# Performance work log

Measured on AMD Instinct MI355X. Metric: run time of the kernel, lower is better.

The kernel has to match this reference:

```python
import math
import jax, jax.numpy as jnp
import numpy as np

# ---- DeepSeek-V2-Lite decoder layer config ----
H = 16            # num_attention_heads
D_NOPE = 128      # qk_nope_head_dim
D_ROPE = 64       # qk_rope_head_dim
D_Q = D_NOPE + D_ROPE  # q_head_dim = 192
D_V = 128         # v_head_dim
KV_RANK = 512     # kv_lora_rank
HID = 2048        # hidden_size
INTER = 10944     # intermediate_size (dense MLP)
MAX_POS = 8192
BASE = 10000.0
FACTOR = 40.0     # yarn scaling factor
ORIG_MAX = 4096
BETA_FAST, BETA_SLOW = 32, 1
MSCALE = 0.707
MSCALE_ALL = 0.707
EPS = 1e-6


def _yarn_cos_sin():
    # DeepseekV2LiteYarnRotaryEmbedding._set_cos_sin_cache
    dim = D_ROPE
    ar = np.arange(0, dim, 2, dtype=np.float32) / dim
    freq_extra = 1.0 / BASE ** ar
    freq_inter = 1.0 / (FACTOR * BASE ** ar)

    def corr_dim(num_rot):
        return dim * math.log(ORIG_MAX / (num_rot * 2 * math.pi)) / (2 * math.log(BASE))

    low = max(math.floor(corr_dim(BETA_FAST)), 0)
    high = min(math.ceil(corr_dim(BETA_SLOW)), dim - 1)
    hi = high + 0.001 if low == high else high
    ramp = np.clip((np.arange(dim // 2, dtype=np.float32) - low) / (hi - low), 0.0, 1.0)
    inv_freq_mask = 1.0 - ramp
    inv_freq = freq_inter * (1 - inv_freq_mask) + freq_extra * inv_freq_mask
    t = np.arange(MAX_POS, dtype=np.float32)
    freqs = np.outer(t, inv_freq)

    def get_mscale(s, m):
        return 1.0 if s <= 1 else 0.1 * m * math.log(s) + 1.0

    ms = get_mscale(FACTOR, MSCALE) / get_mscale(FACTOR, MSCALE_ALL)
    emb = np.concatenate([freqs, freqs], axis=-1)
    return jnp.asarray(np.cos(emb) * ms, jnp.float32), jnp.asarray(np.sin(emb) * ms, jnp.float32)

COS_CACHE, SIN_CACHE = _yarn_cos_sin()  # [MAX_POS, D_ROPE]


def _rms(x, w):
    return x * jax.lax.rsqrt(jnp.mean(x * x, axis=-1, keepdims=True) + EPS) * w


def _deinterleave(x):
    # view(..., d//2, 2).transpose(-1, -2).reshape(..., d)
    d = x.shape[-1]
    return x.reshape(x.shape[:-1] + (d // 2, 2)).swapaxes(-1, -2).reshape(x.shape)


def _apply_rope(x, cos, sin):
    x = _deinterleave(x)
    d = x.shape[-1]
    x1, x2 = x[..., : d // 2], x[..., d // 2:]
    return x * cos + jnp.concatenate([-x2, x1], axis=-1) * sin


def _decoder_layer(hidden_states, position_ids, Wq, Wkva, w_kvln, Wkvb, Wo, Wg, Wu, Wd, w_ln1, w_ln2):
    b, s, _ = hidden_states.shape
    dt = hidden_states.dtype

    # ---- attention block ----
    residual = hidden_states
    x = _rms(hidden_states, w_ln1)

    q = (x @ Wq.T).reshape(b, s, H, D_Q)                 # [b,s,h,192]
    q_nope, q_pe = q[..., :D_NOPE], q[..., D_NOPE:]

    ckv = x @ Wkva.T                                     # [b,s,576]
    c, k_pe = ckv[..., :KV_RANK], ckv[..., KV_RANK:][:, :, None, :]  # [b,s,512],[b,s,1,64]
    kv = (_rms(c, w_kvln) @ Wkvb.T).reshape(b, s, H, D_NOPE + D_V)
    k_nope, v = kv[..., :D_NOPE], kv[..., D_NOPE:]

    cos = COS_CACHE[position_ids][:, :, None, :].astype(dt)  # unsqueeze_dim=2
    sin = SIN_CACHE[position_ids][:, :, None, :].astype(dt)
    q_pe = _apply_rope(q_pe, cos, sin)
    k_pe = _apply_rope(k_pe, cos, sin)

    qf = jnp.concatenate([q_nope, q_pe], axis=-1)                          # [b,s,h,192]
    kf = jnp.concatenate([k_nope, jnp.broadcast_to(k_pe, (b, s, H, D_ROPE))], axis=-1)

    scale = D_Q ** -0.5
    scores = jnp.einsum('bqhd,bkhd->bhqk', qf, kf) * scale
    causal = jnp.tril(jnp.ones((s, s), dtype=bool))
    scores = jnp.where(causal, scores, jnp.finfo(scores.dtype).min)
    probs = jax.nn.softmax(scores, axis=-1)
    attn = jnp.einsum('bhqk,bkhd->bqhd', probs, v).reshape(b, s, H * D_V)
    x = residual + attn @ Wo.T

    # ---- MLP block (SwiGLU) ----
    residual = x
    y = _rms(x, w_ln2)
    x = residual + (jax.nn.silu(y @ Wg.T) * (y @ Wu.T)) @ Wd.T
    return x


def setup_inputs() -> dict:
    key = jax.random.key(0)
    ks = jax.random.split(key, 12)
    B, S = 2, 2048
    sd = 0.02
    inp = {
        'hidden_states': jax.random.normal(ks[0], (B, S, HID), jnp.float32),
        'position_ids': jnp.broadcast_to(jnp.arange(S, dtype=jnp.int32), (B, S)),
        'Wq': jax.random.normal(ks[1], (H * D_Q, HID), jnp.float32) * sd,
        'Wkva': jax.random.normal(ks[2], (KV_RANK + D_ROPE, HID), jnp.float32) * sd,
        'w_kvln': jnp.ones((KV_RANK,), jnp.float32),
        'Wkvb': jax.random.normal(ks[3], (H * (D_NOPE + D_V), KV_RANK), jnp.float32) * sd,
        'Wo': jax.random.normal(ks[4], (HID, H * D_V), jnp.float32) * sd,
        'Wg': jax.random.normal(ks[5], (INTER, HID), jnp.float32) * sd,
        'Wu': jax.random.normal(ks[6], (INTER, HID), jnp.float32) * sd,
        'Wd': jax.random.normal(ks[7], (HID, INTER), jnp.float32) * sd,
        'w_ln1': jnp.ones((HID,), jnp.float32),
        'w_ln2': jnp.ones((HID,), jnp.float32),
    }
    return inp


def reference(hidden_states, position_ids, Wq, Wkva, w_kvln, Wkvb, Wo, Wg, Wu, Wd, w_ln1, w_ln2):
    return _decoder_layer(hidden_states, position_ids, Wq, Wkva, w_kvln, Wkvb, Wo, Wg, Wu, Wd, w_ln1, w_ln2)
```

## Files before the change

### kernel.cpp

```cpp
#include <hip/hip_runtime.h>
#include <hip/hip_bf16.h>
#include <math.h>


typedef short short8 __attribute__((ext_vector_type(8)));
typedef short short4v __attribute__((ext_vector_type(4)));
typedef float f32x4 __attribute__((ext_vector_type(4)));

static __device__ __forceinline__ float bf2f(ushort u) {
  union { uint i; float f; } v; v.i = ((uint)u) << 16; return v.f;
}
static __device__ __forceinline__ ushort f2bf(float x) {
  union { float f; uint i; } v; v.f = x;
  uint r = v.i + 0x7fffu + ((v.i >> 16) & 1u);
  return (ushort)(r >> 16);
}

static __device__ __forceinline__ void glds16(const ushort* g, ushort* l) {
  __builtin_amdgcn_global_load_lds(
      (const __attribute__((address_space(1))) unsigned int*)g,
      (__attribute__((address_space(3))) unsigned int*)l, 16, 0, 0);
}

__global__ __launch_bounds__(256)
void cvt_bf16(const float* __restrict__ in, ushort* __restrict__ out, int n8) {
  int i = blockIdx.x * 256 + threadIdx.x;
  if (i >= n8) return;
  float4 a = ((const float4*)in)[2 * i];
  float4 b = ((const float4*)in)[2 * i + 1];
  short8 o;
  o[0] = (short)f2bf(a.x); o[1] = (short)f2bf(a.y);
  o[2] = (short)f2bf(a.z); o[3] = (short)f2bf(a.w);
  o[4] = (short)f2bf(b.x); o[5] = (short)f2bf(b.y);
  o[6] = (short)f2bf(b.z); o[7] = (short)f2bf(b.w);
  ((short8*)out)[i] = o;
}

__global__ __launch_bounds__(256)
void rms_bf16(const float* __restrict__ in, int istride, int width, float inv_w,
              const float* __restrict__ w, ushort* __restrict__ out, int ostride) {
  const int row = blockIdx.x;
  const float* x = in + (size_t)row * istride;
  float ss = 0.f;
  for (int i = threadIdx.x; i < width; i += 256) { float v = x[i]; ss += v * v; }
#pragma unroll
  for (int off = 32; off > 0; off >>= 1) ss += __shfl_xor(ss, off);
  __shared__ float red[4];
  if ((threadIdx.x & 63) == 0) red[threadIdx.x >> 6] = ss;
  __syncthreads();
  float tot = red[0] + red[1] + red[2] + red[3];
  float scale = rsqrtf(tot * inv_w + 1e-6f);
  ushort* o = out + (size_t)row * ostride;
  for (int i = threadIdx.x; i < width; i += 256) o[i] = f2bf(x[i] * scale * w[i]);
}

template<int EPI>
__global__ __launch_bounds__(256, 2)
void gemm_as(const ushort* __restrict__ A, const ushort* __restrict__ B,
             void* __restrict__ Cv, const void* __restrict__ resv,
             int M, int N, int K) {
  __shared__ ushort As[128 * 32];
  __shared__ ushort Bs[128 * 32];
  const int tid = threadIdx.x;
  const int wave = tid >> 6, lane = tid & 63;
  const int m0 = blockIdx.x * 128, n0 = blockIdx.y * 128;
  const int lm = lane & 15, quad = lane >> 4;
  const int wm = (wave & 1) * 64, wn = (wave >> 1) * 64;

  const int srow = wave * 32 + (lane >> 2);
  const int scol = (lane & 3) * 8;
  const ushort* gA0 = A + (size_t)(m0 + srow) * K + scol;
  const ushort* gA1 = A + (size_t)(m0 + srow + 16) * K + scol;
  int br0 = n0 + srow;      if (br0 > N - 1) br0 = N - 1;
  int br1 = n0 + srow + 16; if (br1 > N - 1) br1 = N - 1;
  const ushort* gB0 = B + (size_t)br0 * K + scol;
  const ushort* gB1 = B + (size_t)br1 * K + scol;
  ushort* lA0 = &As[(wave * 32) * 32];
  ushort* lA1 = &As[(wave * 32 + 16) * 32];
  ushort* lB0 = &Bs[(wave * 32) * 32];
  ushort* lB1 = &Bs[(wave * 32 + 16) * 32];

  f32x4 acc[4][4];
  const f32x4 z4 = {0.f, 0.f, 0.f, 0.f};
#pragma unroll
  for (int i = 0; i < 4; ++i)
#pragma unroll
    for (int j = 0; j < 4; ++j) acc[i][j] = z4;

  for (int k0 = 0; k0 < K; k0 += 32) {
    glds16(gA0 + k0, lA0);
    glds16(gA1 + k0, lA1);
    glds16(gB0 + k0, lB0);
    glds16(gB1 + k0, lB1);
    __syncthreads();

    short8 afr[4], bfr[4];
#pragma unroll
    for (int mt = 0; mt < 4; ++mt)
      afr[mt] = *(const short8*)&As[(wm + mt * 16 + lm) * 32 + quad * 8];
#pragma unroll
    for (int nt = 0; nt < 4; ++nt)
      bfr[nt] = *(const short8*)&Bs[(wn + nt * 16 + lm) * 32 + quad * 8];
#pragma unroll
    for (int mt = 0; mt < 4; ++mt)
#pragma unroll
      for (int nt = 0; nt < 4; ++nt)
        acc[mt][nt] = __builtin_amdgcn_mfma_f32_16x16x32_bf16(
            afr[mt], bfr[nt], acc[mt][nt], 0, 0, 0);
    __syncthreads();
  }

#pragma unroll
  for (int mt = 0; mt < 4; ++mt) {
#pragma unroll
    for (int r = 0; r < 4; ++r) {
      const int grow = m0 + wm + mt * 16 + quad * 4 + r;
#pragma unroll
      for (int nt = 0; nt < 4; ++nt) {
        const int gcol = n0 + wn + nt * 16 + lm;
        if (gcol < N) {
          const size_t idx = (size_t)grow * N + gcol;
          float vacc = acc[mt][nt][r];
          if (EPI == 0) {
            ((ushort*)Cv)[idx] = f2bf(vacc);
          } else if (EPI == 1) {
            ((float*)Cv)[idx] = vacc;
          } else if (EPI == 2) {
            ((float*)Cv)[idx] = vacc + ((const float*)resv)[idx];
          } else {
            float gv = bf2f(((const ushort*)resv)[idx]);
            ((ushort*)Cv)[idx] = f2bf(gv / (1.f + expf(-gv)) * vacc);
          }
        }
      }
    }
  }
}

__global__ __launch_bounds__(64)
void rope_kernel(ushort* __restrict__ q, const float* __restrict__ ckv,
                 const int* __restrict__ pos_ids, ushort* __restrict__ kpe) {
  const int t = blockIdx.x;
  const int j = threadIdx.x;
  const int j2 = j & 31;
  const float ar = (float)j2 * (1.f / 32.f);
  const float fe = exp2f(-ar * 13.287712379549449f);
  const float fi = fe * 0.025f;
  float ramp = ((float)j2 - 10.f) * (1.f / 13.f);
  ramp = fminf(fmaxf(ramp, 0.f), 1.f);
  const float invf = fi * ramp + fe * (1.f - ramp);
  const float ang = (float)pos_ids[t] * invf;
  const float c = cosf(ang), s = sinf(ang);
  const bool lo = j < 32;
  {
    const float* kp = ckv + (size_t)t * 576 + 512;
    float x0 = kp[2 * j2], x1 = kp[2 * j2 + 1];
    float o = lo ? (x0 * c - x1 * s) : (x1 * c + x0 * s);
    kpe[(size_t)t * 64 + j] = f2bf(o);
  }
  for (int h = 0; h < 16; ++h) {
    ushort* qp = q + (size_t)t * 3072 + h * 192 + 128;
    float x0 = bf2f(qp[2 * j2]), x1 = bf2f(qp[2 * j2 + 1]);
    float o = lo ? (x0 * c - x1 * s) : (x1 * c + x0 * s);
    __syncthreads();
    qp[j] = f2bf(o);
  }
}

__global__ __launch_bounds__(256, 2)
void attn_mfma(const ushort* __restrict__ q, const ushort* __restrict__ kv,
               const ushort* __restrict__ kpe, ushort* __restrict__ out) {
  const int qt = (int)gridDim.x - 1 - (int)blockIdx.x;
  const int bh = blockIdx.y;
  const int b = bh >> 4, h = bh & 15;
  const int tid = threadIdx.x;
  const int wave = tid >> 6, lane = tid & 63;
  const int lm = lane & 15, quad = lane >> 4;
  const int wq = wave * 32;
  const float scale = 0.07216878364870323f;

  __shared__ __align__(16) char smem[62464];
  ushort (*Ks)[200] = (ushort(*)[200])smem;
  ushort (*Vt)[72]  = (ushort(*)[72])(smem + 25600);
  ushort (*Pm)[72]  = (ushort(*)[72])(smem + 44032);
  ushort (*Qs)[200] = (ushort(*)[200])smem;

  const size_t tok0 = (size_t)b * 2048;
  const int q0 = qt * 128;

  {
    const ushort* qbase = q + (tok0 + q0) * 3072 + (size_t)h * 192;
#pragma unroll
    for (int it = 0; it < 12; ++it) {
      int idx = (it * 256 + tid) * 8;
      int row = idx / 192, col = idx % 192;
      *(uint4*)&Qs[row][col] = *(const uint4*)(qbase + (size_t)row * 3072 + col);
    }
  }
  __syncthreads();
  short8 qf[2][6];
#pragma unroll
  for (int mt = 0; mt < 2; ++mt)
#pragma unroll
    for (int kk = 0; kk < 6; ++kk)
      qf[mt][kk] = *(const short8*)&Qs[wq + mt * 16 + lm][kk * 32 + quad * 8];
  __syncthreads();

  f32x4 o[2][8];
  const f32x4 z4 = {0.f, 0.f, 0.f, 0.f};
#pragma unroll
  for (int mt = 0; mt < 2; ++mt)
#pragma unroll
    for (int nt = 0; nt < 8; ++nt) o[mt][nt] = z4;
  float m_run[8], l_run[8];
#pragma unroll
  for (int i = 0; i < 8; ++i) { m_run[i] = -3.0e38f; l_run[i] = 0.f; }

  const int nkt = 2 * qt + 2;
  for (int kt = 0; kt < nkt; ++kt) {
    const int kb = kt * 64;
    {
      const int krow = tid >> 2, kq = tid & 3;
      const ushort* src = kv + ((tok0 + kb + krow) * 16 + h) * 256 + kq * 32;
#pragma unroll
      for (int i = 0; i < 4; ++i)
        *(uint4*)&Ks[krow][kq * 32 + i * 8] = *(const uint4*)(src + i * 8);
      const ushort* psrc = kpe + (tok0 + kb + krow) * 64 + kq * 16;
      *(uint4*)&Ks[krow][128 + kq * 16]     = *(const uint4*)(psrc);
      *(uint4*)&Ks[krow][128 + kq * 16 + 8] = *(const uint4*)(psrc + 8);
      const int kgrp = (tid & 15) * 4, dgrp = (tid >> 4) * 8;
      uint4 vv[4];
#pragma unroll
      for (int i = 0; i < 4; ++i)
        vv[i] = *(const uint4*)(kv + ((tok0 + kb + kgrp + i) * 16 + h) * 256 + 128 + dgrp);
#pragma unroll
      for (int j = 0; j < 8; ++j) {
        short4v w;
#pragma unroll
        for (int i = 0; i < 4; ++i) w[i] = (short)((const ushort*)&vv[i])[j];
        *(short4v*)&Vt[dgrp + j][kgrp] = w;
      }
    }
    __syncthreads();

    f32x4 s_acc[2][4];
#pragma unroll
    for (int mt = 0; mt < 2; ++mt)
#pragma unroll
      for (int nt = 0; nt < 4; ++nt) s_acc[mt][nt] = z4;
#pragma unroll
    for (int kk = 0; kk < 6; ++kk) {
      short8 kf[4];
#pragma unroll
      for (int nt = 0; nt < 4; ++nt)
        kf[nt] = *(const short8*)&Ks[nt * 16 + lm][kk * 32 + quad * 8];
#pragma unroll
      for (int mt = 0; mt < 2; ++mt)
#pragma unroll
        for (int nt = 0; nt < 4; ++nt)
          s_acc[mt][nt] = __builtin_amdgcn_mfma_f32_16x16x32_bf16(
              qf[mt][kk], kf[nt], s_acc[mt][nt], 0, 0, 0);
    }

#pragma unroll
    for (int mt = 0; mt < 2; ++mt) {
#pragma unroll
      for (int r = 0; r < 4; ++r) {
        const int qg = q0 + wq + mt * 16 + quad * 4 + r;
        float sv[4];
        float rm = -3.0e38f;
#pragma unroll
        for (int nt = 0; nt < 4; ++nt) {
          const int key = kb + nt * 16 + lm;
          float s = s_acc[mt][nt][r] * scale;
          s = (key <= qg) ? s : -3.0e38f;
          sv[nt] = s;
          rm = fmaxf(rm, s);
        }
#pragma unroll
        for (int off = 1; off < 16; off <<= 1) rm = fmaxf(rm, __shfl_xor(rm, off));
        const int li = mt * 4 + r;
        const float mnew = fmaxf(m_run[li], rm);
        const float alpha = expf(m_run[li] - mnew);
        m_run[li] = mnew;
        float rs = 0.f;
        ushort pb[4];
#pragma unroll
        for (int nt = 0; nt < 4; ++nt) {
          float p = expf(sv[nt] - mnew);
          rs += p;
          pb[nt] = f2bf(p);
        }
#pragma unroll
        for (int off = 1; off < 16; off <<= 1) rs += __shfl_xor(rs, off);
        l_run[li] = l_run[li] * alpha + rs;
#pragma unroll
        for (int nt = 0; nt < 8; ++nt) o[mt][nt][r] *= alpha;
        const int qrow = wq + mt * 16 + quad * 4 + r;
#pragma unroll
        for (int nt = 0; nt < 4; ++nt) Pm[qrow][nt * 16 + lm] = pb[nt];
      }
    }

#pragma unroll
    for (int kt2 = 0; kt2 < 2; ++kt2) {
      short8 pa[2];
#pragma unroll
      for (int mt = 0; mt < 2; ++mt)
        pa[mt] = *(const short8*)&Pm[wq + mt * 16 + lm][kt2 * 32 + quad * 8];
#pragma unroll
      for (int nt = 0; nt < 8; ++nt) {
        short8 vb = *(const short8*)&Vt[nt * 16 + lm][kt2 * 32 + quad * 8];
#pragma unroll
        for (int mt = 0; mt < 2; ++mt)
          o[mt][nt] = __builtin_amdgcn_mfma_f32_16x16x32_bf16(
              pa[mt], vb, o[mt][nt], 0, 0, 0);
      }
    }
    __syncthreads();
  }

  ushort* obase = out + (tok0 + q0) * 2048 + h * 128;
#pragma unroll
  for (int mt = 0; mt < 2; ++mt) {
#pragma unroll
    for (int r = 0; r < 4; ++r) {
      const int qrow = wq + mt * 16 + quad * 4 + r;
      const float inv = 1.f / l_run[mt * 4 + r];
#pragma unroll
      for (int nt = 0; nt < 8; ++nt)
        obase[(size_t)qrow * 2048 + nt * 16 + lm] = f2bf(o[mt][nt][r] * inv);
    }
  }
}

extern "C" void kernel_launch(void* const* d_in, const int* in_sizes, int n_in,
                              void* d_out, int out_size, void* d_ws, size_t ws_size,
                              hipStream_t stream) {
  const float* hidden = (const float*)d_in[0];
  const int*   pos    = (const int*)d_in[1];
  const float* Wq     = (const float*)d_in[2];
  const float* Wkva   = (const float*)d_in[3];
  const float* w_kvln = (const float*)d_in[4];
  const float* Wkvb   = (const float*)d_in[5];
  const float* Wo     = (const float*)d_in[6];
  const float* Wg     = (const float*)d_in[7];
  const float* Wu     = (const float*)d_in[8];
  const float* Wd     = (const float*)d_in[9];
  const float* w_ln1  = (const float*)d_in[10];
  const float* w_ln2  = (const float*)d_in[11];
  float* out = (float*)d_out;

  char* ws = (char*)d_ws;
  ushort* xn    = (ushort*)(ws);
  char*   R1    = ws + 16777216;
  ushort* qb    = (ushort*)(R1);
  float*  ckv   = (float*)(R1 + 25165824);
  ushort* cn    = (ushort*)(R1 + 34603008);
  ushort* kvb   = (ushort*)(R1 + 38797312);
  ushort* kpe   = (ushort*)(R1 + 72351744);
  ushort* attno = (ushort*)(R1 + 72876032);
  ushort* gb    = (ushort*)(R1);
  float*  h1    = (float*)(ws + 196083712);

  char* WSL = ws + 106430464;
  ushort* wq_bf   = (ushort*)(WSL);
  ushort* wkva_bf = (ushort*)(WSL + 12582912);
  ushort* wkvb_bf = (ushort*)(WSL + 14942208);
  ushort* wo_bf   = (ushort*)(WSL + 19136512);
  ushort* wg_bf   = (ushort*)(WSL);
  ushort* wu_bf   = (ushort*)(WSL + 44826624);
  ushort* wd_bf   = (ushort*)(WSL + 44826624);

  cvt_bf16<<<3072, 256, 0, stream>>>(Wq,   wq_bf,   786432);
  cvt_bf16<<<576,  256, 0, stream>>>(Wkva, wkva_bf, 147456);
  cvt_bf16<<<1024, 256, 0, stream>>>(Wkvb, wkvb_bf, 262144);
  cvt_bf16<<<2048, 256, 0, stream>>>(Wo,   wo_bf,   524288);
  cvt_bf16<<<10944, 256, 0, stream>>>(Wu,  wu_bf,   2801664);

  rms_bf16<<<4096, 256, 0, stream>>>(hidden, 2048, 2048, 1.f / 2048.f, w_ln1, xn, 2048);
  gemm_as<0><<<dim3(32, 24), 256, 0, stream>>>(xn, wq_bf, qb, nullptr, 4096, 3072, 2048);
  gemm_as<1><<<dim3(32, 5), 256, 0, stream>>>(xn, wkva_bf, ckv, nullptr, 4096, 576, 2048);
  rms_bf16<<<4096, 256, 0, stream>>>(ckv, 576, 512, 1.f / 512.f, w_kvln, cn, 512);
  gemm_as<0><<<dim3(32, 32), 256, 0, stream>>>(cn, wkvb_bf, kvb, nullptr, 4096, 4096, 512);
  rope_kernel<<<4096, 64, 0, stream>>>(qb, ckv, pos, kpe);
  attn_mfma<<<dim3(16, 32), 256, 0, stream>>>(qb, kvb, kpe, attno);
  gemm_as<2><<<dim3(32, 16), 256, 0, stream>>>(attno, wo_bf, h1, hidden, 4096, 2048, 2048);
  rms_bf16<<<4096, 256, 0, stream>>>(h1, 2048, 2048, 1.f / 2048.f, w_ln2, xn, 2048);

  cvt_bf16<<<10944, 256, 0, stream>>>(Wg, wg_bf, 2801664);
  gemm_as<0><<<dim3(32, 86), 256, 0, stream>>>(xn, wg_bf, gb, nullptr, 4096, 10944, 2048);
  gemm_as<3><<<dim3(32, 86), 256, 0, stream>>>(xn, wu_bf, gb, gb, 4096, 10944, 2048);
  cvt_bf16<<<10944, 256, 0, stream>>>(Wd, wd_bf, 2801664);
  gemm_as<2><<<dim3(32, 16), 256, 0, stream>>>(gb, wd_bf, out, h1, 4096, 2048, 10944);
}
```

Before: 1.522 ms.

## Double GEMM K-tile to 64 with XOR-swizzled LDS layout

Raises the K step of the shared bf16 MFMA GEMM from 32 to 64, so each block does twice as many MFMAs per pair of __syncthreads barriers. It also XOR-swizzles the 16-byte chunks in LDS, using the global source column, so that fragment reads of a 128-byte row spread across banks. LDS use doubles to 32 KB per block, which may limit occupancy at two blocks per CU. K must now be a multiple of 64.

Measured after the change: 1.403 ms. 7.8% less time.

```diff
diff --git a/kernel.cpp b/kernel.cpp
--- a/kernel.cpp
+++ b/kernel.cpp
@@ -59,26 +59,30 @@
 void gemm_as(const ushort* __restrict__ A, const ushort* __restrict__ B,
              void* __restrict__ Cv, const void* __restrict__ resv,
              int M, int N, int K) {
-  __shared__ ushort As[128 * 32];
-  __shared__ ushort Bs[128 * 32];
+  __shared__ ushort As[128 * 64];
+  __shared__ ushort Bs[128 * 64];
   const int tid = threadIdx.x;
   const int wave = tid >> 6, lane = tid & 63;
   const int m0 = blockIdx.x * 128, n0 = blockIdx.y * 128;
   const int lm = lane & 15, quad = lane >> 4;
   const int wm = (wave & 1) * 64, wn = (wave >> 1) * 64;
 
-  const int srow = wave * 32 + (lane >> 2);
-  const int scol = (lane & 3) * 8;
-  const ushort* gA0 = A + (size_t)(m0 + srow) * K + scol;
-  const ushort* gA1 = A + (size_t)(m0 + srow + 16) * K + scol;
-  int br0 = n0 + srow;      if (br0 > N - 1) br0 = N - 1;
-  int br1 = n0 + srow + 16; if (br1 > N - 1) br1 = N - 1;
-  const ushort* gB0 = B + (size_t)br0 * K + scol;
-  const ushort* gB1 = B + (size_t)br1 * K + scol;
-  ushort* lA0 = &As[(wave * 32) * 32];
-  ushort* lA1 = &As[(wave * 32 + 16) * 32];
-  ushort* lB0 = &Bs[(wave * 32) * 32];
-  ushort* lB1 = &Bs[(wave * 32 + 16) * 32];
+  const int lrow = lane >> 3;
+  const int lcq  = lane & 7;
+  const int gu   = lcq ^ lrow;
+  const ushort* gA[4];
+  const ushort* gB[4];
+  ushort* lA[4];
+  ushort* lB[4];
+#pragma unroll
+  for (int j = 0; j < 4; ++j) {
+    const int r = wave * 32 + j * 8 + lrow;
+    gA[j] = A + (size_t)(m0 + r) * K + gu * 8;
+    int br = n0 + r; if (br > N - 1) br = N - 1;
+    gB[j] = B + (size_t)br * K + gu * 8;
+    lA[j] = &As[(wave * 32 + j * 8) * 64];
+    lB[j] = &Bs[(wave * 32 + j * 8) * 64];
+  }
 
   f32x4 acc[4][4];
   const f32x4 z4 = {0.f, 0.f, 0.f, 0.f};
@@ -87,26 +91,32 @@
 #pragma unroll
     for (int j = 0; j < 4; ++j) acc[i][j] = z4;
 
-  for (int k0 = 0; k0 < K; k0 += 32) {
-    glds16(gA0 + k0, lA0);
-    glds16(gA1 + k0, lA1);
-    glds16(gB0 + k0, lB0);
-    glds16(gB1 + k0, lB1);
+  const int sw = lm & 7;
+
+  for (int k0 = 0; k0 < K; k0 += 64) {
+#pragma unroll
+    for (int j = 0; j < 4; ++j) glds16(gA[j] + k0, lA[j]);
+#pragma unroll
+    for (int j = 0; j < 4; ++j) glds16(gB[j] + k0, lB[j]);
     __syncthreads();
 
-    short8 afr[4], bfr[4];
-#pragma unroll
-    for (int mt = 0; mt < 4; ++mt)
-      afr[mt] = *(const short8*)&As[(wm + mt * 16 + lm) * 32 + quad * 8];
-#pragma unroll
-    for (int nt = 0; nt < 4; ++nt)
-      bfr[nt] = *(const short8*)&Bs[(wn + nt * 16 + lm) * 32 + quad * 8];
-#pragma unroll
-    for (int mt = 0; mt < 4; ++mt)
+#pragma unroll
+    for (int kk = 0; kk < 2; ++kk) {
+      const int us = ((kk * 4 + quad) ^ sw) * 8;
+      short8 afr[4], bfr[4];
+#pragma unroll
+      for (int mt = 0; mt < 4; ++mt)
+        afr[mt] = *(const short8*)&As[(wm + mt * 16 + lm) * 64 + us];
 #pragma unroll
       for (int nt = 0; nt < 4; ++nt)
-        acc[mt][nt] = __builtin_amdgcn_mfma_f32_16x16x32_bf16(
-            afr[mt], bfr[nt], acc[mt][nt], 0, 0, 0);
+        bfr[nt] = *(const short8*)&Bs[(wn + nt * 16 + lm) * 64 + us];
+#pragma unroll
+      for (int mt = 0; mt < 4; ++mt)
+#pragma unroll
+        for (int nt = 0; nt < 4; ++nt)
+          acc[mt][nt] = __builtin_amdgcn_mfma_f32_16x16x32_bf16(
+              afr[mt], bfr[nt], acc[mt][nt], 0, 0, 0);
+    }
     __syncthreads();
   }
 
```
